# Kernel tuning notes

Hardware: AMD Instinct MI355X
Metric: run time of the kernel (lower is better)

Reference implementation:

```python
import jax, jax.numpy as jnp
import numpy as np

D_MODEL = 1024
NUM_HEADS = 16
HEAD_DIM = D_MODEL // NUM_HEADS  # 64
D_FF = 4096
EPS = 1e-5


def layer_norm(x, gamma, beta):
    mu = jnp.mean(x, axis=-1, keepdims=True)
    var = jnp.mean((x - mu) ** 2, axis=-1, keepdims=True)
    return (x - mu) * jax.lax.rsqrt(var + EPS) * gamma + beta


def apply_rope(t):
    # t: [B, H, S, head_dim]; interleaved-pair rotation as in RoPE.apply_rope
    S, d = t.shape[-2], t.shape[-1]
    inv_freq = 1.0 / (10000.0 ** (jnp.arange(0, d, 2, dtype=jnp.float32) / d))  # [d/2]
    angles = jnp.arange(S, dtype=jnp.float32)[:, None] * inv_freq[None, :]      # [S, d/2]
    sin, cos = jnp.sin(angles), jnp.cos(angles)
    tp = t.reshape(*t.shape[:-1], d // 2, 2)  # pairs of adjacent elements
    t0, t1 = tp[..., 0], tp[..., 1]
    rot = jnp.stack([t0 * cos - t1 * sin, t0 * sin + t1 * cos], axis=-1)
    return rot.reshape(t.shape)


def setup_inputs() -> dict:
    key = jax.random.key(0)
    ks = jax.random.split(key, 18)
    s = 0.02
    d, f = D_MODEL, D_FF
    return {
        "x": jax.random.normal(ks[0], (2, 2048, d), dtype=jnp.float32),
        "Wq": jax.random.normal(ks[1], (d, d), dtype=jnp.float32) * s,
        "bq": jnp.zeros((d,), jnp.float32),
        "Wk": jax.random.normal(ks[2], (d, d), dtype=jnp.float32) * s,
        "bk": jnp.zeros((d,), jnp.float32),
        "Wv": jax.random.normal(ks[3], (d, d), dtype=jnp.float32) * s,
        "bv": jnp.zeros((d,), jnp.float32),
        "Wo": jax.random.normal(ks[4], (d, d), dtype=jnp.float32) * s,
        "bo": jnp.zeros((d,), jnp.float32),
        "W1": jax.random.normal(ks[5], (d, f), dtype=jnp.float32) * s,
        "b1": jnp.zeros((f,), jnp.float32),
        "W2": jax.random.normal(ks[6], (f, d), dtype=jnp.float32) * s,
        "b2": jnp.zeros((d,), jnp.float32),
        "g1": jnp.ones((d,), jnp.float32),
        "beta1": jnp.zeros((d,), jnp.float32),
        "g2": jnp.ones((d,), jnp.float32),
        "beta2": jnp.zeros((d,), jnp.float32),
    }


def reference(x, Wq, bq, Wk, bk, Wv, bv, Wo, bo, W1, b1, W2, b2, g1, beta1, g2, beta2):
    B, S, d = x.shape
    H, hd = NUM_HEADS, HEAD_DIM
    x_norm = layer_norm(x, g1, beta1)
    q = (x_norm @ Wq + bq).reshape(B, S, H, hd).transpose(0, 2, 1, 3)  # [B,H,S,hd]
    k = (x_norm @ Wk + bk).reshape(B, S, H, hd).transpose(0, 2, 1, 3)
    v = (x_norm @ Wv + bv).reshape(B, S, H, hd).transpose(0, 2, 1, 3)
    q = apply_rope(q)
    k = apply_rope(k)
    q = q * (1.0 / jnp.sqrt(jnp.float32(hd)))
    scores = jnp.einsum("bhqd,bhkd->bhqk", q, k)  # [B,H,S,S]
    attn = jax.nn.softmax(scores, axis=-1)
    out = jnp.einsum("bhqk,bhkd->bhqd", attn, v)
    out = out.transpose(0, 2, 1, 3).reshape(B, S, d)
    attn_out = out @ Wo + bo
    x = x + attn_out  # dropout p=0 (eval)
    x_norm2 = layer_norm(x, g2, beta2)
    ffn = jax.nn.relu(x_norm2 @ W1 + b1) @ W2 + b2
    return x + ffn
```

## Files before the change

kernel.cpp:

```cpp
#include <hip/hip_runtime.h>

typedef unsigned short bf16_t;
typedef short short8 __attribute__((ext_vector_type(8)));
typedef float f32x4 __attribute__((ext_vector_type(4)));
typedef float f32x16 __attribute__((ext_vector_type(16)));
typedef unsigned int u32x4 __attribute__((ext_vector_type(4)));

extern "C" __device__ float __ocml_native_exp2_f32(float);

static __device__ __forceinline__ unsigned short f2bf(float f) {
  unsigned int u = __float_as_uint(f);
  unsigned int r = (u + 0x7FFFu + ((u >> 16) & 1u)) >> 16;
  return (unsigned short)r;
}
static __device__ __forceinline__ float bf2f(unsigned short u) {
  return __uint_as_float((unsigned int)u << 16);
}
static __device__ __forceinline__ unsigned int cvt_pk_bf16(float lo, float hi) {
  unsigned int r;
  asm("v_cvt_pk_bf16_f32 %0, %1, %2" : "=v"(r) : "v"(lo), "v"(hi));
  return r;
}
static __device__ __forceinline__ void pl32swap(unsigned int& a, unsigned int& b) {
  asm("v_permlane32_swap_b32 %0, %1" : "+v"(a), "+v"(b));
}

__device__ __forceinline__ void gload_lds16(const void* g, void* l) {
  __builtin_amdgcn_global_load_lds((const __attribute__((address_space(1))) void*)g,
                                   (__attribute__((address_space(3))) void*)l,
                                   16, 0, 0);
}

__global__ __launch_bounds__(256) void prep_kernel(
    const float* __restrict__ Wq, const float* __restrict__ Wk,
    const float* __restrict__ Wv, const float* __restrict__ Wo,
    const float* __restrict__ W1, const float* __restrict__ W2,
    const float* __restrict__ x, const float* __restrict__ g1,
    const float* __restrict__ be1,
    bf16_t* __restrict__ WqkvT, bf16_t* __restrict__ W1T,
    bf16_t* __restrict__ W2T, bf16_t* __restrict__ xnb) {
  __shared__ float tile[32][33];
  const int bid = blockIdx.x;
  if (bid < 12288) {
    const float* src;
    bf16_t* dst;
    int rows, cols, bx, by;
    if (bid < 4096) {
      const int z = bid >> 10, r = bid & 1023;
      src = (z == 0) ? Wq : (z == 1) ? Wk : (z == 2) ? Wv : Wo;
      dst = WqkvT + (size_t)z * 1048576;
      rows = 1024; cols = 1024;
      bx = (r & 31) * 32; by = (r >> 5) * 32;
    } else if (bid < 8192) {
      const int r = bid - 4096;
      src = W1; dst = W1T; rows = 1024; cols = 4096;
      bx = (r & 127) * 32; by = (r >> 7) * 32;
    } else {
      const int r = bid - 8192;
      src = W2; dst = W2T; rows = 4096; cols = 1024;
      bx = (r & 31) * 32; by = (r >> 5) * 32;
    }
    const int tx = threadIdx.x & 31, ty = threadIdx.x >> 5;
#pragma unroll
    for (int i = 0; i < 32; i += 8)
      tile[ty + i][tx] = src[(size_t)(by + ty + i) * cols + (bx + tx)];
    __syncthreads();
#pragma unroll
    for (int i = 0; i < 32; i += 8)
      dst[(size_t)(bx + ty + i) * rows + (by + tx)] = f2bf(tile[tx][ty + i]);
  } else {
    const int row = bid - 12288;
    const int tid = threadIdx.x;
    const float4 v = reinterpret_cast<const float4*>(x + (size_t)row * 1024)[tid];
    float s = v.x + v.y + v.z + v.w;
    float ss = v.x * v.x + v.y * v.y + v.z * v.z + v.w * v.w;
#pragma unroll
    for (int off = 32; off; off >>= 1) {
      s += __shfl_xor(s, off, 64);
      ss += __shfl_xor(ss, off, 64);
    }
    float* red = &tile[0][0];
    const int wave = tid >> 6, lane = tid & 63;
    if (lane == 0) { red[wave] = s; red[4 + wave] = ss; }
    __syncthreads();
    const float mu = (red[0] + red[1] + red[2] + red[3]) * (1.f / 1024.f);
    const float ms = (red[4] + red[5] + red[6] + red[7]) * (1.f / 1024.f);
    const float rstd = rsqrtf(ms - mu * mu + 1e-5f);
    const float4 gg = reinterpret_cast<const float4*>(g1)[tid];
    const float4 bb = reinterpret_cast<const float4*>(be1)[tid];
    bf16_t* o = xnb + (size_t)row * 1024 + tid * 4;
    o[0] = f2bf((v.x - mu) * rstd * gg.x + bb.x);
    o[1] = f2bf((v.y - mu) * rstd * gg.y + bb.y);
    o[2] = f2bf((v.z - mu) * rstd * gg.z + bb.z);
    o[3] = f2bf((v.w - mu) * rstd * gg.w + bb.w);
  }
}

__global__ __launch_bounds__(256) void ln2_combine(const bf16_t* __restrict__ p,
                                                   const float* __restrict__ x,
                                                   const float* __restrict__ bo,
                                                   const float* __restrict__ g,
                                                   const float* __restrict__ be,
                                                   float* __restrict__ x2,
                                                   bf16_t* __restrict__ xn) {
  const int row = blockIdx.x;
  const int tid = threadIdx.x;
  const float4 xv = reinterpret_cast<const float4*>(x + (size_t)row * 1024)[tid];
  const float4 bb = reinterpret_cast<const float4*>(bo)[tid];
  float4 v = {bb.x + xv.x, bb.y + xv.y, bb.z + xv.z, bb.w + xv.w};
#pragma unroll
  for (int z = 0; z < 4; ++z) {
    const ushort4 a = reinterpret_cast<const ushort4*>(p + (size_t)z * 4194304 + (size_t)row * 1024)[tid];
    v.x += bf2f(a.x); v.y += bf2f(a.y); v.z += bf2f(a.z); v.w += bf2f(a.w);
  }
  reinterpret_cast<float4*>(x2 + (size_t)row * 1024)[tid] = v;
  float s = v.x + v.y + v.z + v.w;
  float ss = v.x * v.x + v.y * v.y + v.z * v.z + v.w * v.w;
#pragma unroll
  for (int off = 32; off; off >>= 1) {
    s += __shfl_xor(s, off, 64);
    ss += __shfl_xor(ss, off, 64);
  }
  __shared__ float red[8];
  const int wave = tid >> 6, lane = tid & 63;
  if (lane == 0) { red[wave] = s; red[4 + wave] = ss; }
  __syncthreads();
  const float mu = (red[0] + red[1] + red[2] + red[3]) * (1.f / 1024.f);
  const float ms = (red[4] + red[5] + red[6] + red[7]) * (1.f / 1024.f);
  const float rstd = rsqrtf(ms - mu * mu + 1e-5f);
  const float4 gg = reinterpret_cast<const float4*>(g)[tid];
  const float4 eb = reinterpret_cast<const float4*>(be)[tid];
  bf16_t* o = xn + (size_t)row * 1024 + tid * 4;
  o[0] = f2bf((v.x - mu) * rstd * gg.x + eb.x);
  o[1] = f2bf((v.y - mu) * rstd * gg.y + eb.y);
  o[2] = f2bf((v.z - mu) * rstd * gg.z + eb.z);
  o[3] = f2bf((v.w - mu) * rstd * gg.w + eb.w);
}

__global__ __launch_bounds__(256) void ffn_combine(const bf16_t* __restrict__ p0,
                                                   const bf16_t* __restrict__ p2,
                                                   const float* __restrict__ x2,
                                                   const float* __restrict__ b2,
                                                   float* __restrict__ out) {
  const int row = blockIdx.x;
  const int tid = threadIdx.x;
  const ushort4 a0 = reinterpret_cast<const ushort4*>(p0 + (size_t)row * 1024)[tid];
  const ushort4 a1 = reinterpret_cast<const ushort4*>(p0 + 4194304 + (size_t)row * 1024)[tid];
  const ushort4 a2 = reinterpret_cast<const ushort4*>(p2 + (size_t)row * 1024)[tid];
  const float4 xv = reinterpret_cast<const float4*>(x2 + (size_t)row * 1024)[tid];
  const float4 bb = reinterpret_cast<const float4*>(b2)[tid];
  float4 v;
  v.x = bf2f(a0.x) + bf2f(a1.x) + bf2f(a2.x) + bb.x + xv.x;
  v.y = bf2f(a0.y) + bf2f(a1.y) + bf2f(a2.y) + bb.y + xv.y;
  v.z = bf2f(a0.z) + bf2f(a1.z) + bf2f(a2.z) + bb.z + xv.z;
  v.w = bf2f(a0.w) + bf2f(a1.w) + bf2f(a2.w) + bb.w + xv.w;
  reinterpret_cast<float4*>(out + (size_t)row * 1024)[tid] = v;
}

__global__ __launch_bounds__(256) void rope_bf16(bf16_t* __restrict__ q,
                                                 bf16_t* __restrict__ k) {
  const int id = blockIdx.x * 256 + threadIdx.x;
  const int i = id & 31;
  const int s = (id >> 5) & 2047;
  const int bh = id >> 16;
  const float inv = exp2f((float)i * -0.41524101186f);
  float sn, cs;
  sincosf((float)s * inv, &sn, &cs);
  const size_t base = ((size_t)bh * 2048 + s) * 64 + 2 * i;
  unsigned int qp = *(unsigned int*)&q[base];
  unsigned int kp = *(unsigned int*)&k[base];
  const float q0 = bf2f(qp & 0xffff), q1 = bf2f(qp >> 16);
  const float k0 = bf2f(kp & 0xffff), k1 = bf2f(kp >> 16);
  const float qs = 0.18033688f;
  const unsigned int qo =
      (unsigned int)f2bf((q0 * cs - q1 * sn) * qs) |
      ((unsigned int)f2bf((q0 * sn + q1 * cs) * qs) << 16);
  const unsigned int ko =
      (unsigned int)f2bf(k0 * cs - k1 * sn) |
      ((unsigned int)f2bf(k0 * sn + k1 * cs) << 16);
  *(unsigned int*)&q[base] = qo;
  *(unsigned int*)&k[base] = ko;
}

__global__ __launch_bounds__(256) void vtrans(const bf16_t* __restrict__ v,
                                              bf16_t* __restrict__ vt) {
  __shared__ bf16_t tile[32][33];
  const int bh = blockIdx.x;
  const int s0 = blockIdx.y * 32;
  const int d0 = blockIdx.z * 32;
  const int tx = threadIdx.x & 31, ty = threadIdx.x >> 5;
  const size_t base = (size_t)bh * (2048 * 64);
#pragma unroll
  for (int i = 0; i < 32; i += 8)
    tile[ty + i][tx] = v[base + (size_t)(s0 + ty + i) * 64 + d0 + tx];
  __syncthreads();
#pragma unroll
  for (int i = 0; i < 32; i += 8)
    vt[base + (size_t)(d0 + ty + i) * 2048 + s0 + tx] = tile[tx][ty + i];
}

__global__ __launch_bounds__(256, 2) void attn7(const bf16_t* __restrict__ qb,
                                                const bf16_t* __restrict__ kb,
                                                const bf16_t* __restrict__ vt,
                                                bf16_t* __restrict__ out) {
  const int bh = blockIdx.x;
  const int tid = threadIdx.x, wave = tid >> 6, lane = tid & 63;
  const int l31 = lane & 31, hi = lane >> 5;
  const int q0 = blockIdx.y * 128 + wave * 32;
  const size_t kvb = (size_t)bh * (2048 * 64);

  __shared__ __align__(16) bf16_t Ks[2][2][4096];
  __shared__ __align__(16) bf16_t Vs[2][2][4096];

  short8 qf[4];
#pragma unroll
  for (int st = 0; st < 4; ++st)
    qf[st] = *(const short8*)&qb[kvb + (size_t)(q0 + l31) * 64 + st * 16 + hi * 8];

  int kidx[2][4];
  int vidx[2][2][2];
#pragma unroll
  for (int st = 0; st < 4; ++st) {
    const int R0 = l31, R1 = 32 + l31;
    kidx[0][st] = (R0 * 8 + (((st << 1) | hi) ^ (R0 & 7))) * 8;
    kidx[1][st] = (R1 * 8 + (((st << 1) | hi) ^ (R1 & 7))) * 8;
  }
#pragma unroll
  for (int f = 0; f < 2; ++f)
#pragma unroll
    for (int ks = 0; ks < 2; ++ks) {
      const int R0 = l31, R1 = 32 + l31;
      vidx[0][f][ks] = (R0 * 8 + (((f << 2) | (ks << 1) | hi) ^ (R0 & 7))) * 8;
      vidx[1][f][ks] = (R1 * 8 + (((f << 2) | (ks << 1) | hi) ^ (R1 & 7))) * 8;
    }

  short8 vones;
#pragma unroll
  for (int j = 0; j < 8; ++j) vones[j] = (short)0x3F80;

  f32x16 acc0 = {}, acc1 = {}, lacc = {};
  const f32x16 fz = {};

#define STAGE(DST, T0)                                                                     \
  {                                                                                        \
    _Pragma("unroll") for (int sub = 0; sub < 2; ++sub) {                                  \
      _Pragma("unroll") for (int j = 0; j < 2; ++j) {                                      \
        const int s = wave * 128 + j * 64 + lane;                                          \
        const int r = s >> 3;                                                              \
        const int c = (s & 7) ^ (r & 7);                                                   \
        gload_lds16(kb + kvb + (size_t)((T0) + sub * 64 + r) * 64 + c * 8,                 \
                    &Ks[DST][sub][(size_t)s * 8]);                                         \
        gload_lds16(vt + kvb + (size_t)r * 2048 + (T0) + sub * 64 + c * 8,                 \
                    &Vs[DST][sub][(size_t)s * 8]);                                         \
      }                                                                                    \
    }                                                                                      \
  }

#define QK(BUF, SUB, P0, P1)                                                               \
  {                                                                                        \
    short8 kfa[4], kfb[4];                                                                 \
    _Pragma("unroll") for (int st = 0; st < 4; ++st) {                                     \
      kfa[st] = *(const short8*)&Ks[BUF][SUB][kidx[0][st]];                                \
      kfb[st] = *(const short8*)&Ks[BUF][SUB][kidx[1][st]];                                \
    }                                                                                      \
    __builtin_amdgcn_s_setprio(1);                                                         \
    P0 = __builtin_amdgcn_mfma_f32_32x32x16_bf16(kfa[0], qf[0], fz, 0, 0, 0);              \
    P1 = __builtin_amdgcn_mfma_f32_32x32x16_bf16(kfb[0], qf[0], fz, 0, 0, 0);              \
    _Pragma("unroll") for (int st = 1; st < 4; ++st) {                                     \
      P0 = __builtin_amdgcn_mfma_f32_32x32x16_bf16(kfa[st], qf[st], P0, 0, 0, 0);          \
      P1 = __builtin_amdgcn_mfma_f32_32x32x16_bf16(kfb[st], qf[st], P1, 0, 0, 0);          \
    }                                                                                      \
    __builtin_amdgcn_s_setprio(0);                                                         \
  }

#define SMPV(BUF, SUB, P0, P1)                                                             \
  {                                                                                        \
    _Pragma("unroll") for (int f = 0; f < 2; ++f) {                                        \
      f32x16& p = f ? P1 : P0;                                                             \
      float e[16];                                                                         \
      _Pragma("unroll") for (int r = 0; r < 16; ++r) e[r] = __ocml_native_exp2_f32(p[r]);  \
      unsigned int a0 = cvt_pk_bf16(e[0], e[1]), b0 = cvt_pk_bf16(e[4], e[5]);             \
      unsigned int a1 = cvt_pk_bf16(e[2], e[3]), b1 = cvt_pk_bf16(e[6], e[7]);             \
      unsigned int a2 = cvt_pk_bf16(e[8], e[9]), b2 = cvt_pk_bf16(e[12], e[13]);           \
      unsigned int a3 = cvt_pk_bf16(e[10], e[11]), b3 = cvt_pk_bf16(e[14], e[15]);         \
      pl32swap(a0, b0);                                                                    \
      pl32swap(a1, b1);                                                                    \
      pl32swap(a2, b2);                                                                    \
      pl32swap(a3, b3);                                                                    \
      const u32x4 w0 = {a0, a1, b0, b1};                                                   \
      const u32x4 w1 = {a2, a3, b2, b3};                                                   \
      const short8 pf0 = __builtin_bit_cast(short8, w0);                                   \
      const short8 pf1 = __builtin_bit_cast(short8, w1);                                   \
      const short8 vf00 = *(const short8*)&Vs[BUF][SUB][vidx[0][f][0]];                    \
      const short8 vf10 = *(const short8*)&Vs[BUF][SUB][vidx[1][f][0]];                    \
      const short8 vf01 = *(const short8*)&Vs[BUF][SUB][vidx[0][f][1]];                    \
      const short8 vf11 = *(const short8*)&Vs[BUF][SUB][vidx[1][f][1]];                    \
      __builtin_amdgcn_s_setprio(1);                                                       \
      lacc = __builtin_amdgcn_mfma_f32_32x32x16_bf16(pf0, vones, lacc, 0, 0, 0);           \
      acc0 = __builtin_amdgcn_mfma_f32_32x32x16_bf16(pf0, vf00, acc0, 0, 0, 0);            \
      acc1 = __builtin_amdgcn_mfma_f32_32x32x16_bf16(pf0, vf10, acc1, 0, 0, 0);            \
      lacc = __builtin_amdgcn_mfma_f32_32x32x16_bf16(pf1, vones, lacc, 0, 0, 0);           \
      acc0 = __builtin_amdgcn_mfma_f32_32x32x16_bf16(pf1, vf01, acc0, 0, 0, 0);            \
      acc1 = __builtin_amdgcn_mfma_f32_32x32x16_bf16(pf1, vf11, acc1, 0, 0, 0);            \
      __builtin_amdgcn_s_setprio(0);                                                       \
    }                                                                                      \
  }

#define CITER(BUF, NT0, DOPREF)                                                            \
  {                                                                                        \
    if (DOPREF) {                                                                          \
      STAGE((BUF) ^ 1, NT0);                                                               \
      asm volatile("s_waitcnt vmcnt(8)" ::: "memory");                                     \
    } else {                                                                               \
      asm volatile("s_waitcnt vmcnt(0)" ::: "memory");                                     \
    }                                                                                      \
    __builtin_amdgcn_s_barrier();                                                          \
    asm volatile("" ::: "memory");                                                         \
    f32x16 pa0, pa1, pb0, pb1;                                                             \
    QK(BUF, 0, pa0, pa1);                                                                  \
    QK(BUF, 1, pb0, pb1);                                                                  \
    SMPV(BUF, 0, pa0, pa1);                                                                \
    SMPV(BUF, 1, pb0, pb1);                                                                \
    asm volatile("" ::: "memory");                                                         \
    __builtin_amdgcn_s_barrier();                                                          \
    asm volatile("" ::: "memory");                                                         \
  }

  STAGE(0, 0);

  for (int k = 0; k < 7; ++k) {
    CITER(0, (2 * k + 1) * 128, 1)
    CITER(1, (2 * k + 2) * 128, 1)
  }
  CITER(0, 1920, 1)
  CITER(1, 0, 0)
#undef CITER
#undef SMPV
#undef QK
#undef STAGE

  const int b = bh >> 4, h = bh & 15;
#pragma unroll
  for (int r = 0; r < 16; ++r) {
    const int qrow = (r & 3) + 8 * (r >> 2) + 4 * hi;
    const float rl = 1.f / lacc[r];
    const size_t ro = (size_t)(b * 2048 + q0 + qrow) * 1024 + h * 64;
    out[ro + l31] = f2bf(acc0[r] * rl);
    out[ro + 32 + l31] = f2bf(acc1[r] * rl);
  }
}

#define SWZ4(r) (((r) ^ ((r) >> 2)) & 3)
#define HP(SL, H) (dynlds + (size_t)(((SL) * 4 + (H)) * 8192))

#define STAGE8(dst, src, row0, kc0)                                             \
  {                                                                             \
    _Pragma("unroll") for (int j = 0; j < 2; ++j) {                             \
      const int s_ = j * 512 + tid;                                             \
      const int r_ = s_ >> 2;                                                   \
      const int c_ = (s_ & 3) ^ SWZ4(r_);                                       \
      gload_lds16(src + (size_t)((row0) + r_) * 1024 + (kc0) + c_ * 8,          \
                  (dst) + (size_t)s_ * 8);                                      \
    }                                                                           \
  }

#define PHASE(SL, KH, MH, STG, VMW)                                             \
  {                                                                             \
    STG;                                                                        \
    short8 af_[4];                                                              \
    _Pragma("unroll") for (int q4 = 0; q4 < 4; ++q4)                            \
      af_[q4] = *(const short8*)(HP(SL, KH) + aidx[(MH) * 4 + q4]);             \
    if ((MH) == 0) {                                                            \
      _Pragma("unroll") for (int ni = 0; ni < 4; ++ni)                          \
        bfr[ni] = *(const short8*)(HP(SL, 2 + (KH)) + bidx[ni]);                \
    }                                                                           \
    VMW;                                                                        \
    asm volatile("" ::: "memory");                                              \
    __builtin_amdgcn_s_barrier();                                               \
    asm volatile("" ::: "memory");                                              \
    __builtin_amdgcn_s_setprio(1);                                              \
    _Pragma("unroll") for (int q4 = 0; q4 < 4; ++q4)                            \
      _Pragma("unroll") for (int ni = 0; ni < 4; ++ni)                          \
        acc[(MH) * 4 + q4][ni] = __builtin_amdgcn_mfma_f32_16x16x32_bf16(       \
            af_[q4], bfr[ni], acc[(MH) * 4 + q4][ni], 0, 0, 0);                 \
    __builtin_amdgcn_s_setprio(0);                                              \
    asm volatile("" ::: "memory");                                              \
    __builtin_amdgcn_s_barrier();                                               \
    asm volatile("" ::: "memory");                                              \
  }

#define KTILE(SL, KT, VM2, VM4)                                                 \
  PHASE(SL, 0, 0,                                                               \
        if ((KT) + 1 < 16) STAGE8(HP((SL) ^ 1, 2), BT, n0, ((KT) + 1) * 64),    \
        (void)0)                                                                \
  PHASE(SL, 0, 1,                                                               \
        if ((KT) + 1 < 16) STAGE8(HP((SL) ^ 1, 1), A, m0, ((KT) + 1) * 64 + 32),\
        asm volatile("s_waitcnt vmcnt(" #VM2 ")" ::: "memory"))                 \
  PHASE(SL, 1, 0,                                                               \
        if ((KT) + 1 < 16) STAGE8(HP((SL) ^ 1, 3), BT, n0, ((KT) + 1) * 64 + 32),\
        (void)0)                                                                \
  PHASE(SL, 1, 1,                                                               \
        if ((KT) + 2 < 16) STAGE8(HP(SL, 0), A, m0, ((KT) + 2) * 64),           \
        asm volatile("s_waitcnt vmcnt(" #VM4 ")" ::: "memory"))

__global__ __launch_bounds__(512, 2) void gemm_ff1_256(
    const bf16_t* __restrict__ A, const bf16_t* __restrict__ BT,
    const float* __restrict__ bias, bf16_t* __restrict__ ob) {
  extern __shared__ bf16_t dynlds[];
  const int tid = threadIdx.x;
  const int wave = tid >> 6, lane = tid & 63;
  const int row16 = lane & 15, quad = lane >> 4;
  const int wr = wave >> 2, wc = wave & 3;
  const int m0 = blockIdx.x * 256, n0 = blockIdx.y * 256;

  int aidx[8], bidx[4];
#pragma unroll
  for (int mi = 0; mi < 8; ++mi) {
    const int R = wr * 128 + mi * 16 + row16;
    aidx[mi] = R * 32 + (quad ^ SWZ4(R)) * 8;
  }
#pragma unroll
  for (int ni = 0; ni < 4; ++ni) {
    const int R = wc * 64 + ni * 16 + row16;
    bidx[ni] = R * 32 + (quad ^ SWZ4(R)) * 8;
  }

  f32x4 acc[8][4];
#pragma unroll
  for (int i = 0; i < 8; ++i)
#pragma unroll
    for (int j = 0; j < 4; ++j) acc[i][j] = (f32x4){0.f, 0.f, 0.f, 0.f};
  short8 bfr[4];

  STAGE8(HP(0, 0), A, m0, 0);
  STAGE8(HP(0, 2), BT, n0, 0);
  STAGE8(HP(0, 1), A, m0, 32);
  STAGE8(HP(0, 3), BT, n0, 32);
  STAGE8(HP(1, 0), A, m0, 64);
  __syncthreads();

  for (int kt2 = 0; kt2 < 7; ++kt2) {
    const int kt = 2 * kt2;
    KTILE(0, kt, 6, 4)
    KTILE(1, kt + 1, 6, 4)
  }
  KTILE(0, 14, 6, 4)
  KTILE(1, 15, 0, 0)

  __syncthreads();
  bf16_t* ct = dynlds;
  float bsv[4];
#pragma unroll
  for (int ni = 0; ni < 4; ++ni) bsv[ni] = bias[n0 + wc * 64 + ni * 16 + row16];
#pragma unroll
  for (int mh = 0; mh < 2; ++mh) {
    if (wr == mh) {
#pragma unroll
      for (int mi = 0; mi < 8; ++mi)
#pragma unroll
        for (int ni = 0; ni < 4; ++ni)
#pragma unroll
          for (int r = 0; r < 4; ++r) {
            const float c = fmaxf(acc[mi][ni][r] + bsv[ni], 0.f);
            ct[(size_t)(mi * 16 + quad * 4 + r) * 264 + wc * 64 + ni * 16 + row16] = f2bf(c);
          }
    }
    __syncthreads();
#pragma unroll
    for (int it = 0; it < 8; ++it) {
      const int u = it * 512 + tid;
      const int lr = u >> 5, lcq = u & 31;
      const uint4 v = *(const uint4*)&ct[(size_t)lr * 264 + lcq * 8];
      *(uint4*)&ob[(size_t)(m0 + mh * 128 + lr) * 4096 + n0 + lcq * 8] = v;
    }
    __syncthreads();
  }
}

enum { MODE_QKV = 0, MODE_FF1 = 1, MODE_PART = 2 };

template <int MODE>
__global__ __launch_bounds__(256) void gemm_bt(
    const bf16_t* __restrict__ A, const bf16_t* __restrict__ BT,
    int M, int N, int K, int kspan,
    const float* __restrict__ bias0, const float* __restrict__ bias1,
    const float* __restrict__ bias2,
    bf16_t* __restrict__ ob0, bf16_t* __restrict__ ob1, bf16_t* __restrict__ ob2) {
  __shared__ __align__(16) char smem[34816];
  bf16_t* As = (bf16_t*)smem;
  bf16_t* Bs = (bf16_t*)(smem + 16384);
  const int tid = threadIdx.x;
  const int wave = tid >> 6, lane = tid & 63;
  const int row16 = lane & 15, quad = lane >> 4;
  const int m0 = blockIdx.x * 128, n0 = blockIdx.y * 128;
  const int wm = (wave & 1) << 6, wn = (wave >> 1) << 6;

  f32x4 acc[4][4];
#pragma unroll
  for (int i = 0; i < 4; ++i)
#pragma unroll
    for (int j = 0; j < 4; ++j) acc[i][j] = (f32x4){0.f, 0.f, 0.f, 0.f};

  const int kb = blockIdx.z * kspan;
  const int kend = (kb + kspan < K) ? kb + kspan : K;

  for (int k0 = kb; k0 < kend; k0 += 64) {
#pragma unroll
    for (int j = 0; j < 4; ++j) {
      const int s = j * 256 + tid;
      const int r = s >> 3;
      const int cg = ((s & 7) ^ (r & 7)) << 3;
      gload_lds16(A + (size_t)(m0 + r) * K + k0 + cg, As + (size_t)s * 8);
      gload_lds16(BT + (size_t)(n0 + r) * K + k0 + cg, Bs + (size_t)s * 8);
    }
    __syncthreads();
    const int sw = row16 & 7;
#pragma unroll
    for (int kk = 0; kk < 2; ++kk) {
      short8 af[4], bfr[4];
#pragma unroll
      for (int mi = 0; mi < 4; ++mi)
        af[mi] = *(const short8*)&As[(size_t)(wm + mi * 16 + row16) * 64 + (((kk << 2) | quad) ^ sw) * 8];
#pragma unroll
      for (int ni = 0; ni < 4; ++ni)
        bfr[ni] = *(const short8*)&Bs[(size_t)(wn + ni * 16 + row16) * 64 + (((kk << 2) | quad) ^ sw) * 8];
#pragma unroll
      for (int mi = 0; mi < 4; ++mi)
#pragma unroll
        for (int ni = 0; ni < 4; ++ni)
          acc[mi][ni] =
              __builtin_amdgcn_mfma_f32_16x16x32_bf16(af[mi], bfr[ni], acc[mi][ni], 0, 0, 0);
    }
    __syncthreads();
  }

  bf16_t* ct = (bf16_t*)smem;
#pragma unroll
  for (int mi = 0; mi < 4; ++mi)
#pragma unroll
    for (int ni = 0; ni < 4; ++ni) {
      const int gn = n0 + wn + ni * 16 + row16;
      float bsv = 0.f;
      if (MODE == MODE_QKV)
        bsv = (gn < 1024) ? bias0[gn] : (gn < 2048) ? bias1[gn - 1024] : bias2[gn - 2048];
      else if (MODE == MODE_FF1)
        bsv = bias0[gn];
#pragma unroll
      for (int r = 0; r < 4; ++r) {
        float c = acc[mi][ni][r] + bsv;
        if (MODE == MODE_FF1) c = fmaxf(c, 0.f);
        ct[(size_t)(wm + mi * 16 + quad * 4 + r) * 136 + wn + ni * 16 + row16] = f2bf(c);
      }
    }
  __syncthreads();
  const int lr0 = tid >> 4, lc = tid & 15;
#pragma unroll
  for (int i = 0; i < 8; ++i) {
    const int lr = i * 16 + lr0;
    const uint4 v = *(const uint4*)&ct[(size_t)lr * 136 + lc * 8];
    const int gm = m0 + lr;
    if (MODE == MODE_QKV) {
      const int nn = (n0 & 1023) + lc * 8;
      const int h = nn >> 6, d = nn & 63;
      const int b = gm >> 11, s = gm & 2047;
      bf16_t* dst = (n0 < 1024) ? ob0 : (n0 < 2048) ? ob1 : ob2;
      *(uint4*)&dst[(((size_t)b * 16 + h) * 2048 + s) * 64 + d] = v;
    } else if (MODE == MODE_FF1) {
      *(uint4*)&ob0[(size_t)gm * N + n0 + lc * 8] = v;
    } else {
      bf16_t* dst = (blockIdx.z == 2) ? ob1 : ob0 + (size_t)blockIdx.z * 4194304;
      *(uint4*)&dst[(size_t)gm * N + n0 + lc * 8] = v;
    }
  }
}

extern "C" void kernel_launch(void* const* d_in, const int* in_sizes, int n_in,
                              void* d_out, int out_size, void* d_ws, size_t ws_size,
                              hipStream_t stream) {
  const float* x = (const float*)d_in[0];
  const float* Wq = (const float*)d_in[1];
  const float* bq = (const float*)d_in[2];
  const float* Wk = (const float*)d_in[3];
  const float* bk = (const float*)d_in[4];
  const float* Wv = (const float*)d_in[5];
  const float* bv = (const float*)d_in[6];
  const float* Wo = (const float*)d_in[7];
  const float* bo = (const float*)d_in[8];
  const float* W1 = (const float*)d_in[9];
  const float* b1 = (const float*)d_in[10];
  const float* W2 = (const float*)d_in[11];
  const float* b2 = (const float*)d_in[12];
  const float* g1 = (const float*)d_in[13];
  const float* be1 = (const float*)d_in[14];
  const float* g2 = (const float*)d_in[15];
  const float* be2 = (const float*)d_in[16];
  float* out = (float*)d_out;

  char* ws = (char*)d_ws;
  size_t off = 0;
  auto alloc = [&](size_t bytes) {
    void* p = ws + off;
    off += (bytes + 255) & ~(size_t)255;
    return p;
  };
  bf16_t* WqkvT = (bf16_t*)alloc(3072ULL * 1024 * 2);
  bf16_t* WoT = (bf16_t*)alloc(1024ULL * 1024 * 2);
  bf16_t* W1T = (bf16_t*)alloc(4096ULL * 1024 * 2);
  bf16_t* W2T = (bf16_t*)alloc(1024ULL * 4096 * 2);
  bf16_t* xnb = (bf16_t*)alloc(4096ULL * 1024 * 2);
  bf16_t* qb = (bf16_t*)alloc(4194304ULL * 2);
  bf16_t* kb = (bf16_t*)alloc(4194304ULL * 2);
  bf16_t* vraw = (bf16_t*)alloc(4194304ULL * 2);
  bf16_t* vt = (bf16_t*)alloc(4194304ULL * 2);
  bf16_t* h1 = qb;
  bf16_t* x2p = qb;
  bf16_t* ffp = WqkvT;
  float* x2 = (float*)alloc(16777216ULL);

  static bool attrset = false;
  if (!attrset) {
    hipFuncSetAttribute((const void*)gemm_ff1_256,
                        hipFuncAttributeMaxDynamicSharedMemorySize, 131072);
    attrset = true;
  }

  prep_kernel<<<16384, 256, 0, stream>>>(Wq, Wk, Wv, Wo, W1, W2, x, g1, be1,
                                         WqkvT, W1T, W2T, xnb);

  gemm_bt<MODE_QKV><<<dim3(32, 24, 1), 256, 0, stream>>>(xnb, WqkvT, 4096, 3072, 1024, 1024,
                                                         bq, bk, bv, qb, kb, vraw);

  rope_bf16<<<8192, 256, 0, stream>>>(qb, kb);

  vtrans<<<dim3(32, 64, 2), 256, 0, stream>>>(vraw, vt);

  attn7<<<dim3(32, 16), 256, 0, stream>>>(qb, kb, vt, xnb);

  gemm_bt<MODE_PART><<<dim3(32, 8, 4), 256, 0, stream>>>(xnb, WoT, 4096, 1024, 1024, 256,
                                                         nullptr, nullptr, nullptr,
                                                         x2p, x2p + 2 * 4194304, nullptr);

  ln2_combine<<<4096, 256, 0, stream>>>(x2p, x, bo, g2, be2, x2, xnb);

  gemm_ff1_256<<<dim3(16, 16), 512, 131072, stream>>>(xnb, W1T, b1, h1);

  gemm_bt<MODE_PART><<<dim3(32, 8, 3), 256, 0, stream>>>(h1, W2T, 4096, 1024, 4096, 1408,
                                                         nullptr, nullptr, nullptr,
                                                         ffp, xnb, nullptr);

  ffn_combine<<<4096, 256, 0, stream>>>(ffp, xnb, x2, b2, out);
}
```

Measured before the change: 344.7 us.

## Fuse RoPE and V transpose into QKV GEMM epilogue with precomputed table

Removes the separate rope_bf16 and vtrans kernels. RoPE rotation and the query scale are now applied in the QKV GEMM epilogue using a sin/cos table computed by extra blocks in prep_kernel. V tiles are written already transposed from shared memory straight to the vt layout. This saves two launches and extra read-write passes over Q, K and V, in exchange for more epilogue work, a table load per output row, and strided shared-memory reads in the V path.

```diff
diff --git a/kernel.cpp b/kernel.cpp
--- a/kernel.cpp
+++ b/kernel.cpp
@@ -38,7 +38,8 @@
     const float* __restrict__ x, const float* __restrict__ g1,
     const float* __restrict__ be1,
     bf16_t* __restrict__ WqkvT, bf16_t* __restrict__ W1T,
-    bf16_t* __restrict__ W2T, bf16_t* __restrict__ xnb) {
+    bf16_t* __restrict__ W2T, bf16_t* __restrict__ xnb,
+    float* __restrict__ ropetbl) {
   __shared__ float tile[32][33];
   const int bid = blockIdx.x;
   if (bid < 12288) {
@@ -68,7 +69,7 @@
 #pragma unroll
     for (int i = 0; i < 32; i += 8)
       dst[(size_t)(bx + ty + i) * rows + (by + tx)] = f2bf(tile[tx][ty + i]);
-  } else {
+  } else if (bid < 16384) {
     const int row = bid - 12288;
     const int tid = threadIdx.x;
     const float4 v = reinterpret_cast<const float4*>(x + (size_t)row * 1024)[tid];
@@ -93,6 +94,12 @@
     o[1] = f2bf((v.y - mu) * rstd * gg.y + bb.y);
     o[2] = f2bf((v.z - mu) * rstd * gg.z + bb.z);
     o[3] = f2bf((v.w - mu) * rstd * gg.w + bb.w);
+  } else {
+    const int id = (bid - 16384) * 256 + threadIdx.x;
+    const int s = id >> 5, i = id & 31;
+    float sn, cs;
+    sincosf((float)s * exp2f((float)i * -0.41524101186f), &sn, &cs);
+    reinterpret_cast<float2*>(ropetbl)[id] = make_float2(cs, sn);
   }
 }
 
@@ -155,48 +162,6 @@
   v.z = bf2f(a0.z) + bf2f(a1.z) + bf2f(a2.z) + bb.z + xv.z;
   v.w = bf2f(a0.w) + bf2f(a1.w) + bf2f(a2.w) + bb.w + xv.w;
   reinterpret_cast<float4*>(out + (size_t)row * 1024)[tid] = v;
-}
-
-__global__ __launch_bounds__(256) void rope_bf16(bf16_t* __restrict__ q,
-                                                 bf16_t* __restrict__ k) {
-  const int id = blockIdx.x * 256 + threadIdx.x;
-  const int i = id & 31;
-  const int s = (id >> 5) & 2047;
-  const int bh = id >> 16;
-  const float inv = exp2f((float)i * -0.41524101186f);
-  float sn, cs;
-  sincosf((float)s * inv, &sn, &cs);
-  const size_t base = ((size_t)bh * 2048 + s) * 64 + 2 * i;
-  unsigned int qp = *(unsigned int*)&q[base];
-  unsigned int kp = *(unsigned int*)&k[base];
-  const float q0 = bf2f(qp & 0xffff), q1 = bf2f(qp >> 16);
-  const float k0 = bf2f(kp & 0xffff), k1 = bf2f(kp >> 16);
-  const float qs = 0.18033688f;
-  const unsigned int qo =
-      (unsigned int)f2bf((q0 * cs - q1 * sn) * qs) |
-      ((unsigned int)f2bf((q0 * sn + q1 * cs) * qs) << 16);
-  const unsigned int ko =
-      (unsigned int)f2bf(k0 * cs - k1 * sn) |
-      ((unsigned int)f2bf(k0 * sn + k1 * cs) << 16);
-  *(unsigned int*)&q[base] = qo;
-  *(unsigned int*)&k[base] = ko;
-}
-
-__global__ __launch_bounds__(256) void vtrans(const bf16_t* __restrict__ v,
-                                              bf16_t* __restrict__ vt) {
-  __shared__ bf16_t tile[32][33];
-  const int bh = blockIdx.x;
-  const int s0 = blockIdx.y * 32;
-  const int d0 = blockIdx.z * 32;
-  const int tx = threadIdx.x & 31, ty = threadIdx.x >> 5;
-  const size_t base = (size_t)bh * (2048 * 64);
-#pragma unroll
-  for (int i = 0; i < 32; i += 8)
-    tile[ty + i][tx] = v[base + (size_t)(s0 + ty + i) * 64 + d0 + tx];
-  __syncthreads();
-#pragma unroll
-  for (int i = 0; i < 32; i += 8)
-    vt[base + (size_t)(d0 + ty + i) * 2048 + s0 + tx] = tile[tx][ty + i];
 }
 
 __global__ __launch_bounds__(256, 2) void attn7(const bf16_t* __restrict__ qb,
@@ -484,7 +449,7 @@
     const bf16_t* __restrict__ A, const bf16_t* __restrict__ BT,
     int M, int N, int K, int kspan,
     const float* __restrict__ bias0, const float* __restrict__ bias1,
-    const float* __restrict__ bias2,
+    const float* __restrict__ bias2, const float* __restrict__ ropetbl,
     bf16_t* __restrict__ ob0, bf16_t* __restrict__ ob1, bf16_t* __restrict__ ob2) {
   __shared__ __align__(16) char smem[34816];
   bf16_t* As = (bf16_t*)smem;
@@ -553,6 +518,31 @@
       }
     }
   __syncthreads();
+
+  if (MODE == MODE_QKV && n0 >= 2048) {
+    const int b = m0 >> 11, sb = m0 & 2047;
+#pragma unroll
+    for (int it = 0; it < 8; ++it) {
+      const int u = it * 256 + tid;
+      const int sg = u & 15, dcol = u >> 4;
+      const int nnv = (n0 - 2048) + dcol;
+      const int h = nnv >> 6, dd = nnv & 63;
+      unsigned short eb[8];
+#pragma unroll
+      for (int k = 0; k < 8; ++k) {
+        const int kk = (k + sg) & 7;
+        eb[kk] = ct[(size_t)(sg * 8 + kk) * 136 + dcol];
+      }
+      uint4 o;
+      o.x = (unsigned)eb[0] | ((unsigned)eb[1] << 16);
+      o.y = (unsigned)eb[2] | ((unsigned)eb[3] << 16);
+      o.z = (unsigned)eb[4] | ((unsigned)eb[5] << 16);
+      o.w = (unsigned)eb[6] | ((unsigned)eb[7] << 16);
+      *(uint4*)&ob2[(((size_t)b * 16 + h) * 64 + dd) * 2048 + sb + sg * 8] = o;
+    }
+    return;
+  }
+
   const int lr0 = tid >> 4, lc = tid & 15;
 #pragma unroll
   for (int i = 0; i < 8; ++i) {
@@ -561,10 +551,27 @@
     const int gm = m0 + lr;
     if (MODE == MODE_QKV) {
       const int nn = (n0 & 1023) + lc * 8;
-      const int h = nn >> 6, d = nn & 63;
+      const int h = nn >> 6, d0 = nn & 63;
+      const int i0 = d0 >> 1;
       const int b = gm >> 11, s = gm & 2047;
-      bf16_t* dst = (n0 < 1024) ? ob0 : (n0 < 2048) ? ob1 : ob2;
-      *(uint4*)&dst[(((size_t)b * 16 + h) * 2048 + s) * 64 + d] = v;
+      const float scale = (n0 < 1024) ? 0.18033688f : 1.0f;
+      const float4 t0 = *(const float4*)&ropetbl[((size_t)s * 32 + i0) * 2];
+      const float4 t1 = *(const float4*)&ropetbl[((size_t)s * 32 + i0) * 2 + 4];
+      const float e0 = bf2f(v.x & 0xffff), e1 = bf2f(v.x >> 16);
+      const float e2 = bf2f(v.y & 0xffff), e3 = bf2f(v.y >> 16);
+      const float e4 = bf2f(v.z & 0xffff), e5 = bf2f(v.z >> 16);
+      const float e6 = bf2f(v.w & 0xffff), e7 = bf2f(v.w >> 16);
+      uint4 o;
+      o.x = (unsigned)f2bf((e0 * t0.x - e1 * t0.y) * scale) |
+            ((unsigned)f2bf((e0 * t0.y + e1 * t0.x) * scale) << 16);
+      o.y = (unsigned)f2bf((e2 * t0.z - e3 * t0.w) * scale) |
+            ((unsigned)f2bf((e2 * t0.w + e3 * t0.z) * scale) << 16);
+      o.z = (unsigned)f2bf((e4 * t1.x - e5 * t1.y) * scale) |
+            ((unsigned)f2bf((e4 * t1.y + e5 * t1.x) * scale) << 16);
+      o.w = (unsigned)f2bf((e6 * t1.z - e7 * t1.w) * scale) |
+            ((unsigned)f2bf((e6 * t1.w + e7 * t1.z) * scale) << 16);
+      bf16_t* dst = (n0 < 1024) ? ob0 : ob1;
+      *(uint4*)&dst[(((size_t)b * 16 + h) * 2048 + s) * 64 + d0] = o;
     } else if (MODE == MODE_FF1) {
       *(uint4*)&ob0[(size_t)gm * N + n0 + lc * 8] = v;
     } else {
@@ -616,6 +623,7 @@
   bf16_t* x2p = qb;
   bf16_t* ffp = WqkvT;
   float* x2 = (float*)alloc(16777216ULL);
+  float* ropetbl = (float*)vraw;
 
   static bool attrset = false;
   if (!attrset) {
@@ -624,20 +632,16 @@
     attrset = true;
   }
 
-  prep_kernel<<<16384, 256, 0, stream>>>(Wq, Wk, Wv, Wo, W1, W2, x, g1, be1,
-                                         WqkvT, W1T, W2T, xnb);
+  prep_kernel<<<16640, 256, 0, stream>>>(Wq, Wk, Wv, Wo, W1, W2, x, g1, be1,
+                                         WqkvT, W1T, W2T, xnb, ropetbl);
 
   gemm_bt<MODE_QKV><<<dim3(32, 24, 1), 256, 0, stream>>>(xnb, WqkvT, 4096, 3072, 1024, 1024,
-                                                         bq, bk, bv, qb, kb, vraw);
-
-  rope_bf16<<<8192, 256, 0, stream>>>(qb, kb);
-
-  vtrans<<<dim3(32, 64, 2), 256, 0, stream>>>(vraw, vt);
+                                                         bq, bk, bv, ropetbl, qb, kb, vt);
 
   attn7<<<dim3(32, 16), 256, 0, stream>>>(qb, kb, vt, xnb);
 
   gemm_bt<MODE_PART><<<dim3(32, 8, 4), 256, 0, stream>>>(xnb, WoT, 4096, 1024, 1024, 256,
-                                                         nullptr, nullptr, nullptr,
+                                                         nullptr, nullptr, nullptr, nullptr,
                                                          x2p, x2p + 2 * 4194304, nullptr);
 
   ln2_combine<<<4096, 256, 0, stream>>>(x2p, x, bo, g2, be2, x2, xnb);
@@ -645,7 +649,7 @@
   gemm_ff1_256<<<dim3(16, 16), 512, 131072, stream>>>(xnb, W1T, b1, h1);
 
   gemm_bt<MODE_PART><<<dim3(32, 8, 3), 256, 0, stream>>>(h1, W2T, 4096, 1024, 4096, 1408,
-                                                         nullptr, nullptr, nullptr,
+                                                         nullptr, nullptr, nullptr, nullptr,
                                                          ffp, xnb, nullptr);
 
   ffn_combine<<<4096, 256, 0, stream>>>(ffp, xnb, x2, b2, out);
```

After: 346.9 us. Within noise of the previous version (+0.6%).
